# Kernel tuning notes

Hardware: AMD Instinct MI355X
Metric: run time of the kernel (lower is better)

Reference implementation:

```python
import jax, jax.numpy as jnp
import numpy as np


def setup_inputs() -> dict:
    key = jax.random.key(0)
    ks = jax.random.split(key, 10)
    b, n, d = 4, 64, 64
    E = 4096
    node_emb = jax.random.normal(ks[0], (b * n, d), dtype=jnp.float32)
    path_emb = jax.random.normal(ks[1], (b, n, n, d), dtype=jnp.float32)
    edge_index = jax.random.randint(ks[2], (2, E), 0, b * n, dtype=jnp.int64)
    # learned params, stored as (in, out) so application is x @ W + b
    W_hz = jax.random.normal(ks[3], (d, d), dtype=jnp.float32) / np.sqrt(d)
    b_hz = jnp.zeros((d,), dtype=jnp.float32)
    W_zz = jax.random.normal(ks[4], (3 * d, d), dtype=jnp.float32) / np.sqrt(3 * d)
    b_zz = jnp.zeros((d,), dtype=jnp.float32)
    W_nm = jax.random.normal(ks[5], (2 * d, d), dtype=jnp.float32) / np.sqrt(2 * d)
    b_nm = jnp.zeros((d,), dtype=jnp.float32)
    return {
        "node_emb": node_emb, "path_emb": path_emb, "edge_index": edge_index,
        "W_hz": W_hz, "b_hz": b_hz, "W_zz": W_zz, "b_zz": b_zz,
        "W_nm": W_nm, "b_nm": b_nm,
    }


def reference(node_emb, path_emb, edge_index, W_hz, b_hz, W_zz, b_zz, W_nm, b_nm):
    b, n, _, d = path_emb.shape
    # ---- PathConv (aggr='max') ----
    z = path_emb @ W_hz + b_hz                                  # (b, n, n, d)
    # tropical (max-plus) matmul over paths: z_conv[b,i,j,d] = max_k z[b,i,k,d] + z[b,k,j,d]
    z_conv = jnp.max(z[:, :, :, None, :] + z[:, None, :, :, :], axis=2)  # (b, n, n, d)
    z = jnp.maximum(z_conv, z)                                  # path_aggr mode='max'
    ne = node_emb.reshape(b, n, d)
    n_i = jnp.broadcast_to(ne[:, :, None, :], (b, n, n, d))
    n_j = jnp.broadcast_to(ne[:, None, :, :], (b, n, n, d))
    u_path = jax.nn.relu(jnp.concatenate([n_i, z, n_j], axis=-1) @ W_zz + b_zz)
    # ---- MPLayer (default message = x_j, aggr='add'; edge_attr unused) ----
    src, dst = edge_index[0], edge_index[1]
    aggr_msg = jax.ops.segment_sum(node_emb[src], dst, num_segments=node_emb.shape[0])
    u_node = jax.nn.relu(jnp.concatenate([node_emb, aggr_msg], axis=-1) @ W_nm + b_nm)
    # residual
    return (u_node + node_emb, u_path + path_emb)
```

## Files before the change

### kernel.cpp

```cpp
#include <hip/hip_runtime.h>


__global__ __launch_bounds__(256) void k_phase1(
    const float* __restrict__ ne, const float* __restrict__ pe,
    const int* __restrict__ eidx,
    const float* __restrict__ Whz, const float* __restrict__ bhz,
    const float* __restrict__ Wzz,
    const float* __restrict__ Wnm, const float* __restrict__ bnm,
    float* __restrict__ zt, float* __restrict__ a1, float* __restrict__ a3,
    float* __restrict__ out0) {
  int bi = blockIdx.x;
  int b  = bi >> 6, i = bi & 63;
  int t = threadIdx.x, lane = t & 63, g = t >> 6;
  __shared__ float sA[64][64];
  __shared__ float sB[64][64];
  __shared__ float sC[64][65];
  __shared__ float part[4][64];
  __shared__ float nl[64], al[64];
  int* elist = (int*)&sA[0][0];

  const float* peb = pe + (size_t)bi * 4096;
  for (int r = g; r < 64; r += 4) {
    sA[r][lane] = peb[r * 64 + lane];
    sB[r][lane] = Whz[r * 64 + lane];
  }
  __syncthreads();
  float acc[16];
  float bv = bhz[lane];
#pragma unroll
  for (int kk = 0; kk < 16; ++kk) acc[kk] = bv;
  int k0 = g * 16;
  for (int c = 0; c < 64; c += 4) {
    float w0 = sB[c + 0][lane], w1 = sB[c + 1][lane];
    float w2 = sB[c + 2][lane], w3 = sB[c + 3][lane];
#pragma unroll
    for (int kk = 0; kk < 16; ++kk) {
      const float4 p = *(const float4*)&sA[k0 + kk][c];
      acc[kk] += p.x * w0 + p.y * w1 + p.z * w2 + p.w * w3;
    }
  }
#pragma unroll
  for (int kk = 0; kk < 16; ++kk) sC[k0 + kk][lane] = acc[kk];
  __syncthreads();
  float* ztb = zt + (size_t)b * 262144 + (size_t)i * 64;
#pragma unroll
  for (int dd = 0; dd < 16; ++dd) {
    int d2 = g * 16 + dd;
    ztb[(size_t)d2 * 4096 + lane] = sC[lane][d2];
  }

  const int* srcv = eidx;
  const int* dstv = eidx + 4096;
  int cntw = 0;
  unsigned long long ltmask = (lane == 63) ? 0x7fffffffffffffffull
                                           : ((1ull << lane) - 1ull);
  for (int q = 0; q < 16; ++q) {
    int e2 = g * 1024 + q * 64 + lane;
    bool match = (dstv[e2] == bi);
    unsigned long long mask = __ballot(match);
    if (match) {
      int pos = cntw + __popcll(mask & ltmask);
      elist[g * 1024 + pos] = srcv[e2];
    }
    cntw += __popcll(mask);
  }
  float accA = 0.f;
  for (int m = 0; m < cntw; ++m) accA += ne[elist[g * 1024 + m] * 64 + lane];
  part[g][lane] = accA;
  if (g == 0) nl[lane] = ne[bi * 64 + lane];
  __syncthreads();
  if (g == 0)
    al[lane] = part[0][lane] + part[1][lane] + part[2][lane] + part[3][lane];
  __syncthreads();
  float s = 0.f;
  for (int d2 = g * 16; d2 < g * 16 + 16; ++d2) {
    s += nl[d2] * Wnm[d2 * 64 + lane] + al[d2] * Wnm[(64 + d2) * 64 + lane];
  }
  part[g][lane] = s;

  if (g == 0) {
    const float* nr = ne + bi * 64;
    float s1 = 0.f;
    for (int d2 = 0; d2 < 64; ++d2) s1 += nr[d2] * Wzz[d2 * 64 + lane];
    a1[bi * 64 + lane] = s1;
  } else if (g == 1) {
    const float* nr = ne + bi * 64;
    float s3 = 0.f;
    for (int d2 = 0; d2 < 64; ++d2) s3 += nr[d2] * Wzz[(128 + d2) * 64 + lane];
    a3[bi * 64 + lane] = s3;
  }
  __syncthreads();
  if (g == 0) {
    float v = part[0][lane] + part[1][lane] + part[2][lane] + part[3][lane]
              + bnm[lane];
    v = fmaxf(v, 0.f);
    out0[bi * 64 + lane] = v + nl[lane];
  }
}

__global__ __launch_bounds__(256) void k_tropical(float* __restrict__ zt) {
  int blk = blockIdx.x;
  float* Ag = zt + (size_t)blk * 4096;
  __shared__ float A[64][64];
  int t = threadIdx.x, lane = t & 63, g = t >> 6;
  {
    const float4* s4 = (const float4*)Ag;
    float4* d4 = (float4*)&A[0][0];
    for (int idx = t; idx < 1024; idx += 256) d4[idx] = s4[idx];
  }
  __syncthreads();
  int j = lane, i0 = g * 16;
  float acc[16];
#pragma unroll
  for (int ii = 0; ii < 16; ++ii) acc[ii] = A[i0 + ii][j];
  for (int k = 0; k < 64; k += 4) {
    float b0 = A[k + 0][j], b1 = A[k + 1][j];
    float b2 = A[k + 2][j], b3 = A[k + 3][j];
#pragma unroll
    for (int ii = 0; ii < 16; ++ii) {
      const float4 a = *(const float4*)&A[i0 + ii][k];
      float m0 = fmaxf(a.x + b0, a.y + b1);
      float m1 = fmaxf(a.z + b2, a.w + b3);
      acc[ii] = fmaxf(acc[ii], fmaxf(m0, m1));
    }
  }
#pragma unroll
  for (int ii = 0; ii < 16; ++ii) Ag[(i0 + ii) * 64 + j] = acc[ii];
}

__global__ __launch_bounds__(256) void k_upath(
    const float* __restrict__ zt, const float* __restrict__ Wzz,
    const float* __restrict__ bzz, const float* __restrict__ a1,
    const float* __restrict__ a3, const float* __restrict__ pe,
    float* __restrict__ out1) {
  int bi = blockIdx.x;
  int b  = bi >> 6;
  int t = threadIdx.x, lane = t & 63, g = t >> 6;
  __shared__ float zf[64][64];
  __shared__ float W2[64][64];
  const float* ztb = zt + (size_t)b * 262144 + (size_t)(bi & 63) * 64;
  for (int d2 = g; d2 < 64; d2 += 4) {
    zf[d2][lane] = ztb[(size_t)d2 * 4096 + lane];
    W2[d2][lane] = Wzz[(64 + d2) * 64 + lane];
  }
  __syncthreads();
  int e = lane, j0 = g * 16;
  float base = a1[bi * 64 + e] + bzz[e];
  float acc[16];
#pragma unroll
  for (int jj = 0; jj < 16; ++jj) acc[jj] = base;
  for (int d2 = 0; d2 < 64; ++d2) {
    float w = W2[d2][e];
#pragma unroll
    for (int jj = 0; jj < 16; jj += 4) {
      const float4 z4 = *(const float4*)&zf[d2][j0 + jj];
      acc[jj + 0] += z4.x * w;
      acc[jj + 1] += z4.y * w;
      acc[jj + 2] += z4.z * w;
      acc[jj + 3] += z4.w * w;
    }
  }
  const float* a3b = a3 + (size_t)(b * 64) * 64;
  size_t obase = (size_t)bi * 4096;
#pragma unroll
  for (int jj = 0; jj < 16; ++jj) {
    int j = j0 + jj;
    float v = acc[jj] + a3b[j * 64 + e];
    v = fmaxf(v, 0.f);
    out1[obase + j * 64 + e] = v + pe[obase + j * 64 + e];
  }
}

extern "C" void kernel_launch(void* const* d_in, const int* in_sizes, int n_in,
                              void* d_out, int out_size, void* d_ws, size_t ws_size,
                              hipStream_t stream) {
  const float* node = (const float*)d_in[0];
  const float* pe   = (const float*)d_in[1];
  const int*   eidx = (const int*)d_in[2];
  const float* Whz  = (const float*)d_in[3];
  const float* bhz  = (const float*)d_in[4];
  const float* Wzz  = (const float*)d_in[5];
  const float* bzz  = (const float*)d_in[6];
  const float* Wnm  = (const float*)d_in[7];
  const float* bnm  = (const float*)d_in[8];
  float* out0 = (float*)d_out;
  float* out1 = out0 + 16384;
  float* zt = (float*)d_ws;
  float* a1 = zt + 4 * 64 * 64 * 64;
  float* a3 = a1 + 256 * 64;

  hipLaunchKernelGGL(k_phase1, dim3(256), dim3(256), 0, stream,
                     node, pe, eidx, Whz, bhz, Wzz, Wnm, bnm, zt, a1, a3, out0);
  hipLaunchKernelGGL(k_tropical, dim3(256), dim3(256), 0, stream, zt);
  hipLaunchKernelGGL(k_upath, dim3(256), dim3(256), 0, stream,
                     zt, Wzz, bzz, a1, a3, pe, out1);
}
```

Measured before the change: 33.92 us.

## Split kernels into quarter-tiles for 4x more blocks and move node work into tropical kernel

Each of the three kernels now launches 1024 blocks instead of 256, with each block handling a quarter of the rows or columns, to fill the GPU's many compute units. The node-message and a1/a3 work moves from the path-linear kernel into extra blocks of the tropical kernel so it runs alongside that stage. The tropical result goes to a separate buffer to avoid in-place hazards between blocks. In exchange, each block reloads full 64x64 weight or z tiles, which adds redundant global-to-LDS traffic, and the scattered float4 stores in k_pathlin are strided.

```diff
diff --git a/kernel.cpp b/kernel.cpp
--- a/kernel.cpp
+++ b/kernel.cpp
@@ -1,170 +1,168 @@
 #include <hip/hip_runtime.h>
 
 
-__global__ __launch_bounds__(256) void k_phase1(
-    const float* __restrict__ ne, const float* __restrict__ pe,
-    const int* __restrict__ eidx,
-    const float* __restrict__ Whz, const float* __restrict__ bhz,
-    const float* __restrict__ Wzz,
-    const float* __restrict__ Wnm, const float* __restrict__ bnm,
-    float* __restrict__ zt, float* __restrict__ a1, float* __restrict__ a3,
-    float* __restrict__ out0) {
-  int bi = blockIdx.x;
-  int b  = bi >> 6, i = bi & 63;
+__global__ __launch_bounds__(256) void k_pathlin(
+    const float* __restrict__ pe, const float* __restrict__ Whz,
+    const float* __restrict__ bhz, float* __restrict__ zt) {
+  int blk = blockIdx.x;
+  int bi = blk >> 2, q = blk & 3;
+  int b = bi >> 6, i = bi & 63;
   int t = threadIdx.x, lane = t & 63, g = t >> 6;
-  __shared__ float sA[64][64];
+  __shared__ float sA[16][64];
   __shared__ float sB[64][64];
-  __shared__ float sC[64][65];
-  __shared__ float part[4][64];
-  __shared__ float nl[64], al[64];
-  int* elist = (int*)&sA[0][0];
-
-  const float* peb = pe + (size_t)bi * 4096;
-  for (int r = g; r < 64; r += 4) {
-    sA[r][lane] = peb[r * 64 + lane];
-    sB[r][lane] = Whz[r * 64 + lane];
+  ((float4*)sA)[t] = ((const float4*)(pe + (size_t)bi * 4096 + q * 1024))[t];
+  {
+    const float4* W4 = (const float4*)Whz;
+    float4* sB4 = (float4*)sB;
+#pragma unroll
+    for (int it = 0; it < 4; ++it) sB4[t + 256 * it] = W4[t + 256 * it];
   }
   __syncthreads();
-  float acc[16];
   float bv = bhz[lane];
-#pragma unroll
-  for (int kk = 0; kk < 16; ++kk) acc[kk] = bv;
-  int k0 = g * 16;
+  float acc[4] = {bv, bv, bv, bv};
+  int kl0 = g * 4;
   for (int c = 0; c < 64; c += 4) {
     float w0 = sB[c + 0][lane], w1 = sB[c + 1][lane];
     float w2 = sB[c + 2][lane], w3 = sB[c + 3][lane];
 #pragma unroll
-    for (int kk = 0; kk < 16; ++kk) {
-      const float4 p = *(const float4*)&sA[k0 + kk][c];
+    for (int kk = 0; kk < 4; ++kk) {
+      const float4 p = *(const float4*)&sA[kl0 + kk][c];
       acc[kk] += p.x * w0 + p.y * w1 + p.z * w2 + p.w * w3;
     }
   }
+  float* dst = zt + (size_t)b * 262144 + (size_t)lane * 4096
+             + (size_t)i * 64 + q * 16 + kl0;
+  *(float4*)dst = make_float4(acc[0], acc[1], acc[2], acc[3]);
+}
+
+__global__ __launch_bounds__(256) void k_trop_node(
+    const float* __restrict__ zt, float* __restrict__ zt2,
+    const float* __restrict__ ne, const int* __restrict__ eidx,
+    const float* __restrict__ Wzz, const float* __restrict__ Wnm,
+    const float* __restrict__ bnm,
+    float* __restrict__ a1, float* __restrict__ a3, float* __restrict__ out0) {
+  int t = threadIdx.x, lane = t & 63, g = t >> 6;
+  __shared__ float A[64][64];
+  __shared__ float part[4][64];
+  __shared__ float nlal[2][64];
+  if (blockIdx.x < 1024) {
+    int slice = blockIdx.x >> 2, iq = blockIdx.x & 3;
+    const float4* s4 = (const float4*)(zt + (size_t)slice * 4096);
+    float4* d4 = (float4*)&A[0][0];
 #pragma unroll
-  for (int kk = 0; kk < 16; ++kk) sC[k0 + kk][lane] = acc[kk];
-  __syncthreads();
-  float* ztb = zt + (size_t)b * 262144 + (size_t)i * 64;
+    for (int it = 0; it < 4; ++it) d4[t + 256 * it] = s4[t + 256 * it];
+    __syncthreads();
+    int j = lane, i0 = iq * 16 + g * 4;
+    float acc[4];
 #pragma unroll
-  for (int dd = 0; dd < 16; ++dd) {
-    int d2 = g * 16 + dd;
-    ztb[(size_t)d2 * 4096 + lane] = sC[lane][d2];
-  }
-
-  const int* srcv = eidx;
-  const int* dstv = eidx + 4096;
-  int cntw = 0;
-  unsigned long long ltmask = (lane == 63) ? 0x7fffffffffffffffull
-                                           : ((1ull << lane) - 1ull);
-  for (int q = 0; q < 16; ++q) {
-    int e2 = g * 1024 + q * 64 + lane;
-    bool match = (dstv[e2] == bi);
-    unsigned long long mask = __ballot(match);
-    if (match) {
-      int pos = cntw + __popcll(mask & ltmask);
-      elist[g * 1024 + pos] = srcv[e2];
+    for (int ii = 0; ii < 4; ++ii) acc[ii] = A[i0 + ii][j];
+    for (int k = 0; k < 64; k += 4) {
+      float b0 = A[k + 0][j], b1 = A[k + 1][j];
+      float b2 = A[k + 2][j], b3 = A[k + 3][j];
+#pragma unroll
+      for (int ii = 0; ii < 4; ++ii) {
+        const float4 a = *(const float4*)&A[i0 + ii][k];
+        float m0 = fmaxf(a.x + b0, a.y + b1);
+        float m1 = fmaxf(a.z + b2, a.w + b3);
+        acc[ii] = fmaxf(acc[ii], fmaxf(m0, m1));
+      }
     }
-    cntw += __popcll(mask);
-  }
-  float accA = 0.f;
-  for (int m = 0; m < cntw; ++m) accA += ne[elist[g * 1024 + m] * 64 + lane];
-  part[g][lane] = accA;
-  if (g == 0) nl[lane] = ne[bi * 64 + lane];
-  __syncthreads();
-  if (g == 0)
-    al[lane] = part[0][lane] + part[1][lane] + part[2][lane] + part[3][lane];
-  __syncthreads();
-  float s = 0.f;
-  for (int d2 = g * 16; d2 < g * 16 + 16; ++d2) {
-    s += nl[d2] * Wnm[d2 * 64 + lane] + al[d2] * Wnm[(64 + d2) * 64 + lane];
-  }
-  part[g][lane] = s;
-
-  if (g == 0) {
-    const float* nr = ne + bi * 64;
-    float s1 = 0.f;
-    for (int d2 = 0; d2 < 64; ++d2) s1 += nr[d2] * Wzz[d2 * 64 + lane];
-    a1[bi * 64 + lane] = s1;
-  } else if (g == 1) {
-    const float* nr = ne + bi * 64;
-    float s3 = 0.f;
-    for (int d2 = 0; d2 < 64; ++d2) s3 += nr[d2] * Wzz[(128 + d2) * 64 + lane];
-    a3[bi * 64 + lane] = s3;
-  }
-  __syncthreads();
-  if (g == 0) {
-    float v = part[0][lane] + part[1][lane] + part[2][lane] + part[3][lane]
-              + bnm[lane];
-    v = fmaxf(v, 0.f);
-    out0[bi * 64 + lane] = v + nl[lane];
+    float* Og = zt2 + (size_t)slice * 4096;
+#pragma unroll
+    for (int ii = 0; ii < 4; ++ii) Og[(i0 + ii) * 64 + j] = acc[ii];
+  } else {
+    int r = blockIdx.x - 1024;
+    int* elist = (int*)&A[0][0];
+    const int* srcv = eidx;
+    const int* dstv = eidx + 4096;
+    int cntw = 0;
+    unsigned long long ltmask = (lane == 63) ? 0x7fffffffffffffffull
+                                             : ((1ull << lane) - 1ull);
+    for (int q = 0; q < 16; ++q) {
+      int e2 = g * 1024 + q * 64 + lane;
+      bool match = (dstv[e2] == r);
+      unsigned long long mask = __ballot(match);
+      if (match) {
+        int pos = cntw + __popcll(mask & ltmask);
+        elist[g * 1024 + pos] = srcv[e2];
+      }
+      cntw += __popcll(mask);
+    }
+    float accA = 0.f;
+    for (int m = 0; m < cntw; ++m) accA += ne[elist[g * 1024 + m] * 64 + lane];
+    part[g][lane] = accA;
+    if (g == 0) nlal[0][lane] = ne[r * 64 + lane];
+    __syncthreads();
+    if (g == 0)
+      nlal[1][lane] = part[0][lane] + part[1][lane] + part[2][lane] + part[3][lane];
+    __syncthreads();
+    float s = 0.f;
+    for (int d2 = g * 16; d2 < g * 16 + 16; ++d2) {
+      s += nlal[0][d2] * Wnm[d2 * 64 + lane]
+         + nlal[1][d2] * Wnm[(64 + d2) * 64 + lane];
+    }
+    part[g][lane] = s;
+    if (g == 0) {
+      const float* nr = ne + r * 64;
+      float s1 = 0.f;
+      for (int d2 = 0; d2 < 64; ++d2) s1 += nr[d2] * Wzz[d2 * 64 + lane];
+      a1[r * 64 + lane] = s1;
+    } else if (g == 1) {
+      const float* nr = ne + r * 64;
+      float s3 = 0.f;
+      for (int d2 = 0; d2 < 64; ++d2) s3 += nr[d2] * Wzz[(128 + d2) * 64 + lane];
+      a3[r * 64 + lane] = s3;
+    }
+    __syncthreads();
+    if (g == 0) {
+      float v = part[0][lane] + part[1][lane] + part[2][lane] + part[3][lane]
+                + bnm[lane];
+      v = fmaxf(v, 0.f);
+      out0[r * 64 + lane] = v + nlal[0][lane];
+    }
   }
 }
 
-__global__ __launch_bounds__(256) void k_tropical(float* __restrict__ zt) {
-  int blk = blockIdx.x;
-  float* Ag = zt + (size_t)blk * 4096;
-  __shared__ float A[64][64];
-  int t = threadIdx.x, lane = t & 63, g = t >> 6;
-  {
-    const float4* s4 = (const float4*)Ag;
-    float4* d4 = (float4*)&A[0][0];
-    for (int idx = t; idx < 1024; idx += 256) d4[idx] = s4[idx];
-  }
-  __syncthreads();
-  int j = lane, i0 = g * 16;
-  float acc[16];
-#pragma unroll
-  for (int ii = 0; ii < 16; ++ii) acc[ii] = A[i0 + ii][j];
-  for (int k = 0; k < 64; k += 4) {
-    float b0 = A[k + 0][j], b1 = A[k + 1][j];
-    float b2 = A[k + 2][j], b3 = A[k + 3][j];
-#pragma unroll
-    for (int ii = 0; ii < 16; ++ii) {
-      const float4 a = *(const float4*)&A[i0 + ii][k];
-      float m0 = fmaxf(a.x + b0, a.y + b1);
-      float m1 = fmaxf(a.z + b2, a.w + b3);
-      acc[ii] = fmaxf(acc[ii], fmaxf(m0, m1));
-    }
-  }
-#pragma unroll
-  for (int ii = 0; ii < 16; ++ii) Ag[(i0 + ii) * 64 + j] = acc[ii];
-}
-
 __global__ __launch_bounds__(256) void k_upath(
-    const float* __restrict__ zt, const float* __restrict__ Wzz,
+    const float* __restrict__ zt2, const float* __restrict__ Wzz,
     const float* __restrict__ bzz, const float* __restrict__ a1,
     const float* __restrict__ a3, const float* __restrict__ pe,
     float* __restrict__ out1) {
-  int bi = blockIdx.x;
-  int b  = bi >> 6;
+  int blk = blockIdx.x;
+  int bi = blk >> 2, jq = blk & 3;
+  int b = bi >> 6, i = bi & 63;
   int t = threadIdx.x, lane = t & 63, g = t >> 6;
-  __shared__ float zf[64][64];
   __shared__ float W2[64][64];
-  const float* ztb = zt + (size_t)b * 262144 + (size_t)(bi & 63) * 64;
-  for (int d2 = g; d2 < 64; d2 += 4) {
-    zf[d2][lane] = ztb[(size_t)d2 * 4096 + lane];
-    W2[d2][lane] = Wzz[(64 + d2) * 64 + lane];
+  __shared__ float sZ[64][16];
+  {
+    const float4* W4 = (const float4*)(Wzz + 4096);
+    float4* W24 = (float4*)W2;
+#pragma unroll
+    for (int it = 0; it < 4; ++it) W24[t + 256 * it] = W4[t + 256 * it];
+  }
+  {
+    int d2 = t >> 2, c4 = t & 3;
+    const float* src = zt2 + (size_t)b * 262144 + (size_t)d2 * 4096
+                     + (size_t)i * 64 + jq * 16 + c4 * 4;
+    *(float4*)&sZ[d2][c4 * 4] = *(const float4*)src;
   }
   __syncthreads();
-  int e = lane, j0 = g * 16;
+  int e = lane;
   float base = a1[bi * 64 + e] + bzz[e];
-  float acc[16];
-#pragma unroll
-  for (int jj = 0; jj < 16; ++jj) acc[jj] = base;
+  float acc[4] = {base, base, base, base};
   for (int d2 = 0; d2 < 64; ++d2) {
     float w = W2[d2][e];
-#pragma unroll
-    for (int jj = 0; jj < 16; jj += 4) {
-      const float4 z4 = *(const float4*)&zf[d2][j0 + jj];
-      acc[jj + 0] += z4.x * w;
-      acc[jj + 1] += z4.y * w;
-      acc[jj + 2] += z4.z * w;
-      acc[jj + 3] += z4.w * w;
-    }
+    const float4 z4 = *(const float4*)&sZ[d2][g * 4];
+    acc[0] += z4.x * w;
+    acc[1] += z4.y * w;
+    acc[2] += z4.z * w;
+    acc[3] += z4.w * w;
   }
   const float* a3b = a3 + (size_t)(b * 64) * 64;
   size_t obase = (size_t)bi * 4096;
 #pragma unroll
-  for (int jj = 0; jj < 16; ++jj) {
-    int j = j0 + jj;
+  for (int jj = 0; jj < 4; ++jj) {
+    int j = jq * 16 + g * 4 + jj;
     float v = acc[jj] + a3b[j * 64 + e];
     v = fmaxf(v, 0.f);
     out1[obase + j * 64 + e] = v + pe[obase + j * 64 + e];
@@ -185,13 +183,14 @@
   const float* bnm  = (const float*)d_in[8];
   float* out0 = (float*)d_out;
   float* out1 = out0 + 16384;
-  float* zt = (float*)d_ws;
-  float* a1 = zt + 4 * 64 * 64 * 64;
-  float* a3 = a1 + 256 * 64;
+  float* zt  = (float*)d_ws;
+  float* a1  = zt + 1048576;
+  float* a3  = a1 + 16384;
+  float* zt2 = a3 + 16384;
 
-  hipLaunchKernelGGL(k_phase1, dim3(256), dim3(256), 0, stream,
-                     node, pe, eidx, Whz, bhz, Wzz, Wnm, bnm, zt, a1, a3, out0);
-  hipLaunchKernelGGL(k_tropical, dim3(256), dim3(256), 0, stream, zt);
-  hipLaunchKernelGGL(k_upath, dim3(256), dim3(256), 0, stream,
-                     zt, Wzz, bzz, a1, a3, pe, out1);
+  hipLaunchKernelGGL(k_pathlin, dim3(1024), dim3(256), 0, stream, pe, Whz, bhz, zt);
+  hipLaunchKernelGGL(k_trop_node, dim3(1280), dim3(256), 0, stream,
+                     zt, zt2, node, eidx, Wzz, Wnm, bnm, a1, a3, out0);
+  hipLaunchKernelGGL(k_upath, dim3(1024), dim3(256), 0, stream,
+                     zt2, Wzz, bzz, a1, a3, pe, out1);
 }
```

Result: faster. 31.45 us (-7.3%).
